# Kernel tuning notes

Hardware: AMD Instinct MI355X
Metric: run time of the kernel (lower is better)

The kernel has to match this reference:

```python
import jax, jax.numpy as jnp
import numpy as np


def setup_inputs() -> dict:
    key = jax.random.key(0)
    k1, k2 = jax.random.split(key)
    B, C, H, W = 8, 64, 128, 256
    left_feature = jax.random.normal(k1, (B, C, H, W), dtype=jnp.float32)
    right_feature = jax.random.normal(k2, (B, C, H, W), dtype=jnp.float32)
    return {
        "left_feature": left_feature,
        "right_feature": right_feature,
        "max_disp": 64,
    }


def reference(left_feature, right_feature, max_disp):
    # Stereo correlation cost volume (norm=False branch):
    #   volume[b, d, h, w] = mean_c( left[b,c,h,w] * right[b,c,h,w-d] )  for w >= d
    #   volume[b, d, h, w] = 0                                           for w <  d
    b, c, h, w = left_feature.shape

    def corr_at_disp(d):
        # left[:, :, :, d:] * right[:, :, :, :w-d], mean over channel dim
        prod = left_feature[:, :, :, d:] * right_feature[:, :, :, : w - d]
        cv = jnp.mean(prod, axis=1)  # (b, h, w-d)
        # left-pad along width with zeros for invalid disparities
        return jnp.pad(cv, ((0, 0), (0, 0), (d, 0)))

    # max_disp is a static Python int; loop over disparity hyperparameter is static.
    volume = jnp.stack([corr_at_disp(d) for d in range(max_disp)], axis=1)
    return volume  # (b, max_disp, h, w)
```

## Files before the change

### kernel.cpp

```cpp
#include <hip/hip_runtime.h>

typedef _Float16 half8 __attribute__((ext_vector_type(8)));
typedef float floatx4 __attribute__((ext_vector_type(4)));

#define BB 8
#define CC 64
#define HH 128
#define WW 256
#define DD 64
#define NROW 2
#define GRID 512
#define OPITCH 260

__global__ __launch_bounds__(512, 2)
void corr_volume_mfma(const float* __restrict__ left,
                      const float* __restrict__ right,
                      float* __restrict__ out) {
    __shared__ alignas(16) unsigned char smem[73728];
    _Float16* const Lb = (_Float16*)smem;
    _Float16* const Rb = (_Float16*)(smem + 32768);
    float*    const Ob = (float*)smem;

    const int tid  = threadIdx.x;
    const int lane = tid & 63;
    const int wv   = tid >> 6;
    const int sw   = lane * 4;
    const int cg   = wv;

    const size_t chanStride = (size_t)HH * WW;

    float4 lv[8], rv[8];

    {
        const int bh = blockIdx.x;
        const size_t rowBase = (size_t)(bh >> 7) * CC * chanStride
                             + (size_t)(bh & 127) * WW;
        const float* lp = left  + rowBase + (size_t)(cg * 8) * chanStride + sw;
        const float* rp = right + rowBase + (size_t)(cg * 8) * chanStride + sw;
        #pragma unroll
        for (int c = 0; c < 8; ++c) {
            lv[c] = *(const float4*)(lp + (size_t)c * chanStride);
            rv[c] = *(const float4*)(rp + (size_t)c * chanStride);
        }
    }

    const int n = lane & 15;
    const int q = lane >> 4;
    const int wbase = wv * 32;
    const float scale = 1.0f / 64.0f;

    #pragma unroll
    for (int k = 0; k < NROW; ++k) {
        const int bh = blockIdx.x + k * GRID;
        const int b  = bh >> 7;
        const int h  = bh & 127;

        __syncthreads();

        {
            half8 z = {0, 0, 0, 0, 0, 0, 0, 0};
            *(half8*)&Rb[tid * 8] = z;
        }

        {
            const float* lf = (const float*)lv;
            const float* rf = (const float*)rv;
            #pragma unroll
            for (int s = 0; s < 4; ++s) {
                const int w   = sw + s;
                const int col = (cg ^ (w & 7)) * 8;
                half8 lh, rh;
                #pragma unroll
                for (int c = 0; c < 8; ++c) {
                    lh[c] = (_Float16)lf[c * 4 + s];
                    rh[c] = (_Float16)rf[c * 4 + s];
                }
                *(half8*)&Lb[w * 64 + col]        = lh;
                *(half8*)&Rb[(w + 64) * 64 + col] = rh;
            }
        }
        __syncthreads();

        floatx4 acc[2][5];
        #pragma unroll
        for (int t = 0; t < 2; ++t)
            #pragma unroll
            for (int u = 0; u < 5; ++u)
                #pragma unroll
                for (int r = 0; r < 4; ++r)
                    acc[t][u][r] = 0.0f;

        #pragma unroll
        for (int kk = 0; kk < 2; ++kk) {
            const int col = ((kk * 4 + q) ^ (n & 7)) * 8;
            half8 bfrag[2], afrag[6];
            #pragma unroll
            for (int t = 0; t < 2; ++t)
                bfrag[t] = *(const half8*)&Lb[(wbase + t * 16 + n) * 64 + col];
            #pragma unroll
            for (int a = 0; a < 6; ++a)
                afrag[a] = *(const half8*)&Rb[(wbase + a * 16 + n) * 64 + col];
            #pragma unroll
            for (int t = 0; t < 2; ++t)
                #pragma unroll
                for (int u = 0; u < 5; ++u)
                    acc[t][u] = __builtin_amdgcn_mfma_f32_16x16x32_f16(
                        afrag[t + u], bfrag[t], acc[t][u], 0, 0, 0);
        }
        __syncthreads();

        #pragma unroll
        for (int t = 0; t < 2; ++t) {
            const int w = wbase + t * 16 + n;
            #pragma unroll
            for (int u = 0; u < 5; ++u) {
                #pragma unroll
                for (int r = 0; r < 4; ++r) {
                    const int d = 64 - 16 * u + n - (q * 4 + r);
                    if (d >= 0 && d < DD) {
                        Ob[d * OPITCH + w] = acc[t][u][r] * scale;
                    }
                }
            }
        }
        __syncthreads();

        if (k + 1 < NROW) {
            const int bh2 = blockIdx.x + (k + 1) * GRID;
            const size_t rowBase2 = (size_t)(bh2 >> 7) * CC * chanStride
                                  + (size_t)(bh2 & 127) * WW;
            const float* lp = left  + rowBase2 + (size_t)(cg * 8) * chanStride + sw;
            const float* rp = right + rowBase2 + (size_t)(cg * 8) * chanStride + sw;
            #pragma unroll
            for (int c = 0; c < 8; ++c) {
                lv[c] = *(const float4*)(lp + (size_t)c * chanStride);
                rv[c] = *(const float4*)(rp + (size_t)c * chanStride);
            }
        }

        #pragma unroll
        for (int i = 0; i < 8; ++i) {
            const int d = wv * 8 + i;
            const float4 v = *(const float4*)&Ob[d * OPITCH + lane * 4];
            *(float4*)&out[(((size_t)b * DD + d) * HH + h) * WW + lane * 4] = v;
        }
    }
}

extern "C" void kernel_launch(void* const* d_in, const int* in_sizes, int n_in,
                              void* d_out, int out_size, void* d_ws, size_t ws_size,
                              hipStream_t stream) {
    const float* left  = (const float*)d_in[0];
    const float* right = (const float*)d_in[1];
    float* out = (float*)d_out;

    dim3 grid(GRID);
    dim3 block(512);
    corr_volume_mfma<<<grid, block, 0, stream>>>(left, right, out);
}
```

Baseline: 171.9 us.

## Split work into single-wave blocks per 32-column strip with halo loads

Replaces 512-thread blocks that each process two full rows with 8192 single-wavefront blocks, each handling a 32-wide output strip of one row. Each block loads its own right-feature halo (up to 64 columns back) and zero-pads invalid columns, so blocks are independent and need much less shared memory. Block indices are swizzled so neighbouring strips land on different blocks. The change trades extra redundant right-feature loads (up to three times) and more block launches for finer-grained scheduling and higher occupancy.

New measurement: 184.8 us. 1.08x slower.

```diff
diff --git a/kernel.cpp b/kernel.cpp
--- a/kernel.cpp
+++ b/kernel.cpp
@@ -8,142 +8,172 @@
 #define HH 128
 #define WW 256
 #define DD 64
-#define NROW 2
-#define GRID 512
-#define OPITCH 260
+#define OPITCH 36
 
-__global__ __launch_bounds__(512, 2)
+__global__ __launch_bounds__(64, 3)
 void corr_volume_mfma(const float* __restrict__ left,
                       const float* __restrict__ right,
                       float* __restrict__ out) {
-    __shared__ alignas(16) unsigned char smem[73728];
+    __shared__ alignas(16) unsigned char smem[16384];
     _Float16* const Lb = (_Float16*)smem;
-    _Float16* const Rb = (_Float16*)(smem + 32768);
+    _Float16* const Rb = (_Float16*)(smem + 4096);
     float*    const Ob = (float*)smem;
 
-    const int tid  = threadIdx.x;
-    const int lane = tid & 63;
-    const int wv   = tid >> 6;
-    const int sw   = lane * 4;
-    const int cg   = wv;
+    const int lane = threadIdx.x;
+
+    const int tsk = (blockIdx.x & 7) * 1024 + (blockIdx.x >> 3);
+    const int bh  = tsk >> 3;
+    const int W0  = (tsk & 7) * 32;
+    const int b   = bh >> 7;
+    const int h   = bh & 127;
 
     const size_t chanStride = (size_t)HH * WW;
+    const size_t rowBase = (size_t)b * CC * chanStride + (size_t)h * WW;
 
-    float4 lv[8], rv[8];
+    const int cg = lane >> 3;
+    const int wq = (lane & 7) * 4;
+
+    const float* lp = left  + rowBase + (size_t)(cg * 8) * chanStride;
+    const float* rp = right + rowBase + (size_t)(cg * 8) * chanStride;
+
+    float4 lv[8], ra[8], rbv[8];
+
+    #pragma unroll
+    for (int c = 0; c < 8; ++c)
+        lv[c] = *(const float4*)(lp + (size_t)c * chanStride + (W0 + wq));
+    #pragma unroll
+    for (int c = 0; c < 8; ++c)
+        ra[c] = *(const float4*)(rp + (size_t)c * chanStride + (W0 + wq));
+
+    if (W0 < 64) {
+        const int nz8 = (64 - W0) * 8;
+        half8 z = {0, 0, 0, 0, 0, 0, 0, 0};
+        for (int zz = lane; zz < nz8; zz += 64)
+            *(half8*)&Rb[zz * 8] = z;
+    }
 
     {
-        const int bh = blockIdx.x;
-        const size_t rowBase = (size_t)(bh >> 7) * CC * chanStride
-                             + (size_t)(bh & 127) * WW;
-        const float* lp = left  + rowBase + (size_t)(cg * 8) * chanStride + sw;
-        const float* rp = right + rowBase + (size_t)(cg * 8) * chanStride + sw;
+        const float* lf = (const float*)lv;
         #pragma unroll
-        for (int c = 0; c < 8; ++c) {
-            lv[c] = *(const float4*)(lp + (size_t)c * chanStride);
-            rv[c] = *(const float4*)(rp + (size_t)c * chanStride);
+        for (int s = 0; s < 4; ++s) {
+            const int j   = wq + s;
+            const int col = (cg ^ (j & 7)) * 8;
+            half8 v;
+            #pragma unroll
+            for (int c = 0; c < 8; ++c) v[c] = (_Float16)lf[c * 4 + s];
+            *(half8*)&Lb[j * 64 + col] = v;
         }
     }
 
+    if (W0 >= 32) {
+        #pragma unroll
+        for (int c = 0; c < 8; ++c)
+            rbv[c] = *(const float4*)(rp + (size_t)c * chanStride + (W0 - 32 + wq));
+    }
+
+    {
+        const float* rf = (const float*)ra;
+        #pragma unroll
+        for (int s = 0; s < 4; ++s) {
+            const int j   = 64 + wq + s;
+            const int col = (cg ^ (j & 7)) * 8;
+            half8 v;
+            #pragma unroll
+            for (int c = 0; c < 8; ++c) v[c] = (_Float16)rf[c * 4 + s];
+            *(half8*)&Rb[j * 64 + col] = v;
+        }
+    }
+
+    if (W0 >= 64) {
+        #pragma unroll
+        for (int c = 0; c < 8; ++c)
+            ra[c] = *(const float4*)(rp + (size_t)c * chanStride + (W0 - 64 + wq));
+    }
+
+    if (W0 >= 32) {
+        const float* rf = (const float*)rbv;
+        #pragma unroll
+        for (int s = 0; s < 4; ++s) {
+            const int j   = 32 + wq + s;
+            const int col = (cg ^ (j & 7)) * 8;
+            half8 v;
+            #pragma unroll
+            for (int c = 0; c < 8; ++c) v[c] = (_Float16)rf[c * 4 + s];
+            *(half8*)&Rb[j * 64 + col] = v;
+        }
+    }
+
+    if (W0 >= 64) {
+        const float* rf = (const float*)ra;
+        #pragma unroll
+        for (int s = 0; s < 4; ++s) {
+            const int j   = wq + s;
+            const int col = (cg ^ (j & 7)) * 8;
+            half8 v;
+            #pragma unroll
+            for (int c = 0; c < 8; ++c) v[c] = (_Float16)rf[c * 4 + s];
+            *(half8*)&Rb[j * 64 + col] = v;
+        }
+    }
+
+    __syncthreads();
+
     const int n = lane & 15;
     const int q = lane >> 4;
-    const int wbase = wv * 32;
     const float scale = 1.0f / 64.0f;
 
+    floatx4 acc[2][5];
     #pragma unroll
-    for (int k = 0; k < NROW; ++k) {
-        const int bh = blockIdx.x + k * GRID;
-        const int b  = bh >> 7;
-        const int h  = bh & 127;
+    for (int tt = 0; tt < 2; ++tt)
+        #pragma unroll
+        for (int u = 0; u < 5; ++u)
+            #pragma unroll
+            for (int r = 0; r < 4; ++r)
+                acc[tt][u][r] = 0.0f;
 
-        __syncthreads();
-
-        {
-            half8 z = {0, 0, 0, 0, 0, 0, 0, 0};
-            *(half8*)&Rb[tid * 8] = z;
-        }
-
-        {
-            const float* lf = (const float*)lv;
-            const float* rf = (const float*)rv;
-            #pragma unroll
-            for (int s = 0; s < 4; ++s) {
-                const int w   = sw + s;
-                const int col = (cg ^ (w & 7)) * 8;
-                half8 lh, rh;
-                #pragma unroll
-                for (int c = 0; c < 8; ++c) {
-                    lh[c] = (_Float16)lf[c * 4 + s];
-                    rh[c] = (_Float16)rf[c * 4 + s];
-                }
-                *(half8*)&Lb[w * 64 + col]        = lh;
-                *(half8*)&Rb[(w + 64) * 64 + col] = rh;
-            }
-        }
-        __syncthreads();
-
-        floatx4 acc[2][5];
+    #pragma unroll
+    for (int kk = 0; kk < 2; ++kk) {
+        const int col = ((kk * 4 + q) ^ (n & 7)) * 8;
+        half8 bfrag[2], afrag[6];
         #pragma unroll
-        for (int t = 0; t < 2; ++t)
+        for (int tt = 0; tt < 2; ++tt)
+            bfrag[tt] = *(const half8*)&Lb[(tt * 16 + n) * 64 + col];
+        #pragma unroll
+        for (int a = 0; a < 6; ++a)
+            afrag[a] = *(const half8*)&Rb[(a * 16 + n) * 64 + col];
+        #pragma unroll
+        for (int tt = 0; tt < 2; ++tt)
             #pragma unroll
             for (int u = 0; u < 5; ++u)
-                #pragma unroll
-                for (int r = 0; r < 4; ++r)
-                    acc[t][u][r] = 0.0f;
+                acc[tt][u] = __builtin_amdgcn_mfma_f32_16x16x32_f16(
+                    afrag[tt + u], bfrag[tt], acc[tt][u], 0, 0, 0);
+    }
 
+    __syncthreads();
+
+    #pragma unroll
+    for (int tt = 0; tt < 2; ++tt) {
+        const int wloc = tt * 16 + n;
         #pragma unroll
-        for (int kk = 0; kk < 2; ++kk) {
-            const int col = ((kk * 4 + q) ^ (n & 7)) * 8;
-            half8 bfrag[2], afrag[6];
+        for (int u = 0; u < 5; ++u) {
             #pragma unroll
-            for (int t = 0; t < 2; ++t)
-                bfrag[t] = *(const half8*)&Lb[(wbase + t * 16 + n) * 64 + col];
-            #pragma unroll
-            for (int a = 0; a < 6; ++a)
-                afrag[a] = *(const half8*)&Rb[(wbase + a * 16 + n) * 64 + col];
-            #pragma unroll
-            for (int t = 0; t < 2; ++t)
-                #pragma unroll
-                for (int u = 0; u < 5; ++u)
-                    acc[t][u] = __builtin_amdgcn_mfma_f32_16x16x32_f16(
-                        afrag[t + u], bfrag[t], acc[t][u], 0, 0, 0);
-        }
-        __syncthreads();
-
-        #pragma unroll
-        for (int t = 0; t < 2; ++t) {
-            const int w = wbase + t * 16 + n;
-            #pragma unroll
-            for (int u = 0; u < 5; ++u) {
-                #pragma unroll
-                for (int r = 0; r < 4; ++r) {
-                    const int d = 64 - 16 * u + n - (q * 4 + r);
-                    if (d >= 0 && d < DD) {
-                        Ob[d * OPITCH + w] = acc[t][u][r] * scale;
-                    }
+            for (int r = 0; r < 4; ++r) {
+                const int d = 64 - 16 * u + n - (q * 4 + r);
+                if (d >= 0 && d < DD) {
+                    Ob[d * OPITCH + wloc] = acc[tt][u][r] * scale;
                 }
             }
         }
-        __syncthreads();
+    }
 
-        if (k + 1 < NROW) {
-            const int bh2 = blockIdx.x + (k + 1) * GRID;
-            const size_t rowBase2 = (size_t)(bh2 >> 7) * CC * chanStride
-                                  + (size_t)(bh2 & 127) * WW;
-            const float* lp = left  + rowBase2 + (size_t)(cg * 8) * chanStride + sw;
-            const float* rp = right + rowBase2 + (size_t)(cg * 8) * chanStride + sw;
-            #pragma unroll
-            for (int c = 0; c < 8; ++c) {
-                lv[c] = *(const float4*)(lp + (size_t)c * chanStride);
-                rv[c] = *(const float4*)(rp + (size_t)c * chanStride);
-            }
-        }
+    __syncthreads();
 
-        #pragma unroll
-        for (int i = 0; i < 8; ++i) {
-            const int d = wv * 8 + i;
-            const float4 v = *(const float4*)&Ob[d * OPITCH + lane * 4];
-            *(float4*)&out[(((size_t)b * DD + d) * HH + h) * WW + lane * 4] = v;
-        }
+    #pragma unroll
+    for (int ii = 0; ii < 8; ++ii) {
+        const int d    = ii * 8 + (lane >> 3);
+        const int wloc = (lane & 7) * 4;
+        const float4 v = *(const float4*)&Ob[d * OPITCH + wloc];
+        *(float4*)&out[(((size_t)b * DD + d) * HH + h) * WW + W0 + wloc] = v;
     }
 }
 
@@ -154,7 +184,7 @@
     const float* right = (const float*)d_in[1];
     float* out = (float*)d_out;
 
-    dim3 grid(GRID);
-    dim3 block(512);
+    dim3 grid(8192);
+    dim3 block(64);
     corr_volume_mfma<<<grid, block, 0, stream>>>(left, right, out);
 }
```

## Split each row into half-width tiles with per-wave output staging

Applied to the files above, without the earlier changes.

Each block now handles half of a row's width with 256 threads, and the grid doubles to 1024 blocks. The right-half tile loads a 64-column halo of the right feature so it can compute disparities near its left edge. The output transpose is staged in per-wave LDS slices, which removes one block-wide barrier, and the LDS swizzle becomes a two-level XOR to avoid bank conflicts. A block-index swizzle spreads work across XCDs. The aim is higher occupancy and less synchronisation, at the cost of redundant halo loads and uneven work between the two halves.

Measured after the change: 193.2 us. 1.12x slower.

```diff
diff --git a/kernel.cpp b/kernel.cpp
--- a/kernel.cpp
+++ b/kernel.cpp
@@ -1,6 +1,7 @@
 #include <hip/hip_runtime.h>
 
-typedef _Float16 half8 __attribute__((ext_vector_type(8)));
+typedef _Float16 half8_t __attribute__((ext_vector_type(8)));
+typedef _Float16 half4_t __attribute__((ext_vector_type(4)));
 typedef float floatx4 __attribute__((ext_vector_type(4)));
 
 #define BB 8
@@ -9,74 +10,102 @@
 #define WW 256
 #define DD 64
 #define NROW 2
-#define GRID 512
-#define OPITCH 260
+#define GRID 1024
+#define OPITCH 36
 
-__global__ __launch_bounds__(512, 2)
+__global__ __launch_bounds__(256, 4)
 void corr_volume_mfma(const float* __restrict__ left,
                       const float* __restrict__ right,
                       float* __restrict__ out) {
-    __shared__ alignas(16) unsigned char smem[73728];
+    __shared__ alignas(16) unsigned char smem[40960];
     _Float16* const Lb = (_Float16*)smem;
-    _Float16* const Rb = (_Float16*)(smem + 32768);
-    float*    const Ob = (float*)smem;
+    _Float16* const Rb = (_Float16*)(smem + 16384);
 
     const int tid  = threadIdx.x;
     const int lane = tid & 63;
     const int wv   = tid >> 6;
-    const int sw   = lane * 4;
-    const int cg   = wv;
+    float* const Obw = (float*)smem + wv * (DD * OPITCH);
+
+    const int swz = (blockIdx.x & 7) * 128 + (blockIdx.x >> 3);
+    const int hf  = swz & 1;
+    const int W0  = hf << 7;
 
     const size_t chanStride = (size_t)HH * WW;
 
-    float4 lv[8], rv[8];
+    const int cg  = tid >> 5;
+    const int wq  = (tid & 31) * 4;
+    const int cg4 = tid >> 4;
+    const int wq4 = (tid & 15) * 4;
+
+    float4 lv[8], ra[8], rb4[4];
 
     {
-        const int bh = blockIdx.x;
+        const int bh = swz >> 1;
         const size_t rowBase = (size_t)(bh >> 7) * CC * chanStride
                              + (size_t)(bh & 127) * WW;
-        const float* lp = left  + rowBase + (size_t)(cg * 8) * chanStride + sw;
-        const float* rp = right + rowBase + (size_t)(cg * 8) * chanStride + sw;
+        const float* lp = left  + rowBase + (size_t)(cg * 8) * chanStride + W0 + wq;
+        const float* rp = right + rowBase + (size_t)(cg * 8) * chanStride + W0 + wq;
         #pragma unroll
-        for (int c = 0; c < 8; ++c) {
-            lv[c] = *(const float4*)(lp + (size_t)c * chanStride);
-            rv[c] = *(const float4*)(rp + (size_t)c * chanStride);
+        for (int c = 0; c < 8; ++c) lv[c] = *(const float4*)(lp + (size_t)c * chanStride);
+        #pragma unroll
+        for (int c = 0; c < 8; ++c) ra[c] = *(const float4*)(rp + (size_t)c * chanStride);
+        if (hf) {
+            const float* rq = right + rowBase + (size_t)(cg4 * 4) * chanStride + (W0 - 64) + wq4;
+            #pragma unroll
+            for (int c = 0; c < 4; ++c) rb4[c] = *(const float4*)(rq + (size_t)c * chanStride);
         }
     }
 
-    const int n = lane & 15;
-    const int q = lane >> 4;
+    const int n  = lane & 15;
+    const int qd = lane >> 4;
     const int wbase = wv * 32;
     const float scale = 1.0f / 64.0f;
 
     #pragma unroll
     for (int k = 0; k < NROW; ++k) {
-        const int bh = blockIdx.x + k * GRID;
-        const int b  = bh >> 7;
-        const int h  = bh & 127;
+        const int tsk = swz + k * GRID;
+        const int bh  = tsk >> 1;
+        const int b   = bh >> 7;
+        const int h   = bh & 127;
 
         __syncthreads();
 
-        {
-            half8 z = {0, 0, 0, 0, 0, 0, 0, 0};
-            *(half8*)&Rb[tid * 8] = z;
+        if (!hf) {
+            half8_t z = {0, 0, 0, 0, 0, 0, 0, 0};
+            *(half8_t*)&Rb[tid * 16]     = z;
+            *(half8_t*)&Rb[tid * 16 + 8] = z;
         }
 
         {
             const float* lf = (const float*)lv;
-            const float* rf = (const float*)rv;
+            const float* rf = (const float*)ra;
             #pragma unroll
             for (int s = 0; s < 4; ++s) {
-                const int w   = sw + s;
-                const int col = (cg ^ (w & 7)) * 8;
-                half8 lh, rh;
+                const int jl = wq + s;
+                const int cl = (cg ^ (jl & 7) ^ ((jl >> 3) & 7)) * 8;
+                const int jr = jl + 64;
+                const int cr = (cg ^ (jr & 7) ^ ((jr >> 3) & 7)) * 8;
+                half8_t vL, vR;
                 #pragma unroll
                 for (int c = 0; c < 8; ++c) {
-                    lh[c] = (_Float16)lf[c * 4 + s];
-                    rh[c] = (_Float16)rf[c * 4 + s];
+                    vL[c] = (_Float16)lf[c * 4 + s];
+                    vR[c] = (_Float16)rf[c * 4 + s];
                 }
-                *(half8*)&Lb[w * 64 + col]        = lh;
-                *(half8*)&Rb[(w + 64) * 64 + col] = rh;
+                *(half8_t*)&Lb[jl * 64 + cl] = vL;
+                *(half8_t*)&Rb[jr * 64 + cr] = vR;
+            }
+            if (hf) {
+                const float* rg = (const float*)rb4;
+                #pragma unroll
+                for (int s = 0; s < 4; ++s) {
+                    const int j  = wq4 + s;
+                    const int cb = ((cg4 >> 1) ^ (j & 7) ^ ((j >> 3) & 7)) * 8
+                                 + (cg4 & 1) * 4;
+                    half4_t v;
+                    #pragma unroll
+                    for (int c = 0; c < 4; ++c) v[c] = (_Float16)rg[c * 4 + s];
+                    *(half4_t*)&Rb[j * 64 + cb] = v;
+                }
             }
         }
         __syncthreads();
@@ -92,14 +121,18 @@
 
         #pragma unroll
         for (int kk = 0; kk < 2; ++kk) {
-            const int col = ((kk * 4 + q) ^ (n & 7)) * 8;
-            half8 bfrag[2], afrag[6];
+            const int xb = (kk * 4 + qd) ^ (n & 7);
+            half8_t bfrag[2], afrag[6];
             #pragma unroll
-            for (int t = 0; t < 2; ++t)
-                bfrag[t] = *(const half8*)&Lb[(wbase + t * 16 + n) * 64 + col];
+            for (int t = 0; t < 2; ++t) {
+                const int j = wbase + t * 16 + n;
+                bfrag[t] = *(const half8_t*)&Lb[j * 64 + (xb ^ ((j >> 3) & 7)) * 8];
+            }
             #pragma unroll
-            for (int a = 0; a < 6; ++a)
-                afrag[a] = *(const half8*)&Rb[(wbase + a * 16 + n) * 64 + col];
+            for (int a = 0; a < 6; ++a) {
+                const int j = wbase + a * 16 + n;
+                afrag[a] = *(const half8_t*)&Rb[j * 64 + (xb ^ ((j >> 3) & 7)) * 8];
+            }
             #pragma unroll
             for (int t = 0; t < 2; ++t)
                 #pragma unroll
@@ -111,38 +144,42 @@
 
         #pragma unroll
         for (int t = 0; t < 2; ++t) {
-            const int w = wbase + t * 16 + n;
+            const int wl = t * 16 + n;
             #pragma unroll
             for (int u = 0; u < 5; ++u) {
                 #pragma unroll
                 for (int r = 0; r < 4; ++r) {
-                    const int d = 64 - 16 * u + n - (q * 4 + r);
+                    const int d = 64 - 16 * u + n - (qd * 4 + r);
                     if (d >= 0 && d < DD) {
-                        Ob[d * OPITCH + w] = acc[t][u][r] * scale;
+                        Obw[d * OPITCH + wl] = acc[t][u][r] * scale;
                     }
                 }
             }
         }
-        __syncthreads();
 
         if (k + 1 < NROW) {
-            const int bh2 = blockIdx.x + (k + 1) * GRID;
+            const int bh2 = (swz + (k + 1) * GRID) >> 1;
             const size_t rowBase2 = (size_t)(bh2 >> 7) * CC * chanStride
                                   + (size_t)(bh2 & 127) * WW;
-            const float* lp = left  + rowBase2 + (size_t)(cg * 8) * chanStride + sw;
-            const float* rp = right + rowBase2 + (size_t)(cg * 8) * chanStride + sw;
+            const float* lp = left  + rowBase2 + (size_t)(cg * 8) * chanStride + W0 + wq;
+            const float* rp = right + rowBase2 + (size_t)(cg * 8) * chanStride + W0 + wq;
             #pragma unroll
-            for (int c = 0; c < 8; ++c) {
-                lv[c] = *(const float4*)(lp + (size_t)c * chanStride);
-                rv[c] = *(const float4*)(rp + (size_t)c * chanStride);
+            for (int c = 0; c < 8; ++c) lv[c] = *(const float4*)(lp + (size_t)c * chanStride);
+            #pragma unroll
+            for (int c = 0; c < 8; ++c) ra[c] = *(const float4*)(rp + (size_t)c * chanStride);
+            if (hf) {
+                const float* rq = right + rowBase2 + (size_t)(cg4 * 4) * chanStride + (W0 - 64) + wq4;
+                #pragma unroll
+                for (int c = 0; c < 4; ++c) rb4[c] = *(const float4*)(rq + (size_t)c * chanStride);
             }
         }
 
         #pragma unroll
         for (int i = 0; i < 8; ++i) {
-            const int d = wv * 8 + i;
-            const float4 v = *(const float4*)&Ob[d * OPITCH + lane * 4];
-            *(float4*)&out[(((size_t)b * DD + d) * HH + h) * WW + lane * 4] = v;
+            const int d  = i * 8 + (lane >> 3);
+            const int wl = (lane & 7) * 4;
+            const float4 v = *(const float4*)&Obw[d * OPITCH + wl];
+            *(float4*)&out[(((size_t)b * DD + d) * HH + h) * WW + W0 + wbase + wl] = v;
         }
     }
 }
@@ -155,6 +192,6 @@
     float* out = (float*)d_out;
 
     dim3 grid(GRID);
-    dim3 block(512);
+    dim3 block(256);
     corr_volume_mfma<<<grid, block, 0, stream>>>(left, right, out);
 }
```
